# Kernel tuning notes

Measured on AMD Instinct MI355X. Metric: run time of the kernel, lower is better.

Reference implementation:

```python
import jax, jax.numpy as jnp
import numpy as np

T, B, C = 1024, 16, 1024
H, K, PAD_L = 16, 7, 3  # num_heads, kernel_size, padding_l
OUT = 1024


def setup_inputs() -> dict:
    key = jax.random.key(0)
    ks = jax.random.split(key, 8)
    s_in = 1.0 / np.sqrt(C)
    return {
        "x": jax.random.normal(ks[0], (T, B, C), dtype=jnp.float32),
        "W1": jax.random.normal(ks[1], (C, C), dtype=jnp.float32) * s_in,
        "b1": jnp.zeros((C,), dtype=jnp.float32),
        "Wq": jax.random.normal(ks[2], (C, H * K), dtype=jnp.float32) * s_in,
        "bq": jnp.zeros((H * K,), dtype=jnp.float32),
        "conv_bias": jax.random.normal(ks[3], (C,), dtype=jnp.float32) * 0.02,
        "W2": jax.random.normal(ks[4], (C, OUT), dtype=jnp.float32) * s_in,
        "b2": jnp.zeros((OUT,), dtype=jnp.float32),
    }


def reference(x, W1, b1, Wq, bq, conv_bias, W2, b2):
    # linear1 (glu=False -> no activation)
    h = x @ W1 + b1                       # [T, B, C]
    Tn, Bn, Cn = h.shape
    R = Cn // H                           # channels per head
    # dynamic filter prediction from query (= h), softmax over K taps
    w = (h @ Wq + bq).reshape(Tn, Bn, H, K)
    w = jax.nn.softmax(w, axis=-1)        # [T, B, H, K]
    # unfold1d: pad PAD_L left, K-1-PAD_L right along time, gather K-windows
    hp = jnp.pad(h, ((PAD_L, K - 1 - PAD_L), (0, 0), (0, 0)))
    win = jnp.stack([hp[k:k + Tn] for k in range(K)], axis=-1)  # [T, B, C, K]
    win = win.reshape(Tn, Bn, H, R, K)
    out = jnp.einsum('tbhrk,tbhk->tbhr', win, w).reshape(Tn, Bn, Cn)
    out = out + conv_bias                 # [T, B, C]
    return out @ W2 + b2                  # [T, B, OUT]
```

## Files before the change

kernel.cpp:

```cpp
#include <hip/hip_runtime.h>
#include <math.h>

#define T_DIM 1024
#define B_DIM 16
#define C_DIM 1024
#define H_DIM 16
#define K_TAPS 7
#define PAD_LEFT 3
#define OUT_DIM 1024
#define M_DIM (T_DIM * B_DIM)
#define HK 112
#define HKP 128
#define KD 1024
#define NT32 (KD / 32)

typedef __attribute__((ext_vector_type(8))) short bf16x8;
typedef __attribute__((ext_vector_type(4))) float f32x4;

__device__ __forceinline__ ushort f2bf(float f) {
    union { float f; unsigned u; } v; v.f = f;
    unsigned u = v.u;
    u += 0x7fffu + ((u >> 16) & 1u);
    return (ushort)(u >> 16);
}
__device__ __forceinline__ float bf2f(ushort h) {
    union { unsigned u; float f; } v; v.u = ((unsigned)h) << 16;
    return v.f;
}

__global__ __launch_bounds__(256) void cvt_bf16x8(const float* __restrict__ in,
                                                  ushort* __restrict__ out,
                                                  int n8) {
    int i = blockIdx.x * blockDim.x + threadIdx.x;
    if (i >= n8) return;
    const float4* p = (const float4*)in;
    float4 a = p[2 * i], b = p[2 * i + 1];
    uint4 o;
    o.x = (unsigned)f2bf(a.x) | ((unsigned)f2bf(a.y) << 16);
    o.y = (unsigned)f2bf(a.z) | ((unsigned)f2bf(a.w) << 16);
    o.z = (unsigned)f2bf(b.x) | ((unsigned)f2bf(b.y) << 16);
    o.w = (unsigned)f2bf(b.z) | ((unsigned)f2bf(b.w) << 16);
    ((uint4*)out)[i] = o;
}

__global__ void transpose_cvt(const float* __restrict__ W,
                              ushort* __restrict__ Wt,
                              int Kd, int N, int Npad) {
    __shared__ float tile[32][33];
    int n0 = blockIdx.x * 32, k0 = blockIdx.y * 32;
    int tx = threadIdx.x, ty = threadIdx.y;
#pragma unroll
    for (int j = 0; j < 4; ++j) {
        int k = k0 + ty * 4 + j;
        int n = n0 + tx;
        tile[ty * 4 + j][tx] = (n < N) ? W[(size_t)k * N + n] : 0.f;
    }
    __syncthreads();
#pragma unroll
    for (int j = 0; j < 4; ++j) {
        int n = n0 + ty * 4 + j;
        if (n < Npad)
            Wt[(size_t)n * Kd + k0 + tx] = f2bf(tile[tx][ty * 4 + j]);
    }
}

template <bool OUT_BF16>
__global__ __launch_bounds__(256, 2) void gemm_k32(
    const ushort* __restrict__ A, const ushort* __restrict__ Bt,
    const float* __restrict__ bias, void* __restrict__ Cp, int ldc) {
    __shared__ ushort Ab[2][256 * 32];
    __shared__ ushort Bb[2][128 * 32];

    const int tid  = threadIdx.x;
    const int lane = tid & 63;
    const int wid  = tid >> 6;
    const int wr = wid >> 1;
    const int wc = wid & 1;
    const int fr = lane & 15;
    const int fq = lane >> 4;

    const int orig = blockIdx.x;
    const int nid  = (orig & 7) * 64 + (orig >> 3);
    const int bm = (nid >> 3) * 256;
    const int bn = (nid & 7) * 128;

    const int rA   = tid >> 2;
    const int slA  = (tid & 3) * 8;
    const size_t srcA0 = (size_t)(bm + rA) * KD + slA;
    const size_t srcB0 = (size_t)(bn + rA) * KD + slA;

    const int aBase0 = (wr * 128 + fr) * 32 + fq * 8;
    const int bBase0 = (wc * 64 + fr) * 32 + fq * 8;

    f32x4 acc[8][4];
#pragma unroll
    for (int m = 0; m < 8; ++m)
#pragma unroll
        for (int n = 0; n < 4; ++n) acc[m][n] = (f32x4){0.f, 0.f, 0.f, 0.f};

    auto stage = [&](int buf, int t) {
        const ushort* Ap = A + srcA0 + t * 32;
        const ushort* Bp = Bt + srcB0 + t * 32;
#pragma unroll
        for (int i = 0; i < 4; ++i)
            __builtin_amdgcn_global_load_lds(
                (const __attribute__((address_space(1))) void*)(Ap + (size_t)i * 64 * KD),
                (__attribute__((address_space(3))) void*)(&Ab[buf][(i * 256 + wid * 64) * 8]),
                16, 0, 0);
#pragma unroll
        for (int i = 0; i < 2; ++i)
            __builtin_amdgcn_global_load_lds(
                (const __attribute__((address_space(1))) void*)(Bp + (size_t)i * 64 * KD),
                (__attribute__((address_space(3))) void*)(&Bb[buf][(i * 256 + wid * 64) * 8]),
                16, 0, 0);
    };

    stage(0, 0);
    stage(1, 1);
    asm volatile("s_waitcnt vmcnt(6)" ::: "memory");
    __builtin_amdgcn_sched_barrier(0);
    __builtin_amdgcn_s_barrier();

#pragma unroll 1
    for (int t = 0; t < NT32; ++t) {
        const int cur = t & 1;
        const ushort* Ac = &Ab[cur][0];
        const ushort* Bc = &Bb[cur][0];

        bf16x8 a[8], b[4];
#pragma unroll
        for (int n = 0; n < 4; ++n)
            b[n] = *(const bf16x8*)(Bc + bBase0 + n * 512);
#pragma unroll
        for (int m = 0; m < 8; ++m)
            a[m] = *(const bf16x8*)(Ac + aBase0 + m * 512);

        asm volatile("s_waitcnt lgkmcnt(0)" ::: "memory");
        __builtin_amdgcn_sched_barrier(0);
        __builtin_amdgcn_s_barrier();

        if (t < NT32 - 2) stage(cur, t + 2);

        __builtin_amdgcn_s_setprio(1);
#pragma unroll
        for (int m = 0; m < 8; ++m)
#pragma unroll
            for (int n = 0; n < 4; ++n)
                acc[m][n] = __builtin_amdgcn_mfma_f32_16x16x32_bf16(
                    a[m], b[n], acc[m][n], 0, 0, 0);
        __builtin_amdgcn_s_setprio(0);

        if (t < NT32 - 2) {
            asm volatile("s_waitcnt vmcnt(6)" ::: "memory");
        } else if (t == NT32 - 2) {
            asm volatile("s_waitcnt vmcnt(0)" ::: "memory");
        }
        __builtin_amdgcn_sched_barrier(0);
        if (t < NT32 - 1) __builtin_amdgcn_s_barrier();
    }

#pragma unroll
    for (int n = 0; n < 4; ++n) {
        int col = bn + wc * 64 + n * 16 + fr;
        float bv = bias[col];
#pragma unroll
        for (int m = 0; m < 8; ++m) {
#pragma unroll
            for (int r = 0; r < 4; ++r) {
                int row = bm + wr * 128 + m * 16 + fq * 4 + r;
                float v = acc[m][n][r] + bv;
                if (OUT_BF16)
                    ((ushort*)Cp)[(size_t)row * ldc + col] = f2bf(v);
                else
                    ((float*)Cp)[(size_t)row * ldc + col] = v;
            }
        }
    }
}

template <bool OUT_BF16, bool NGUARD>
__global__ __launch_bounds__(256) void gemm_mfma(const ushort* __restrict__ A,
                                                 const ushort* __restrict__ Bt,
                                                 const float* __restrict__ bias,
                                                 void* __restrict__ Cp,
                                                 int Kd, int N, int ldc) {
    __shared__ ushort Als[128 * 32];
    __shared__ ushort Bls[128 * 32];
    const int tid  = threadIdx.x;
    const int lane = tid & 63;
    const int wid  = tid >> 6;
    const int wr = wid >> 1, wc = wid & 1;
    const int bm = blockIdx.y * 128, bn = blockIdx.x * 128;
    const int fq = lane >> 4, fr = lane & 15;

    f32x4 acc[4][4];
#pragma unroll
    for (int m = 0; m < 4; ++m)
#pragma unroll
        for (int n = 0; n < 4; ++n) acc[m][n] = (f32x4){0.f, 0.f, 0.f, 0.f};

    const int c0 = wid * 128 + lane;
    const int c1 = c0 + 64;
    const int r0 = c0 >> 2, o0 = (c0 & 3) * 8;
    const int r1 = c1 >> 2, o1 = (c1 & 3) * 8;

    for (int k0 = 0; k0 < Kd; k0 += 32) {
        __builtin_amdgcn_global_load_lds(
            (const __attribute__((address_space(1))) void*)&A[(size_t)(bm + r0) * Kd + k0 + o0],
            (__attribute__((address_space(3))) void*)&Als[(wid * 2 + 0) * 512], 16, 0, 0);
        __builtin_amdgcn_global_load_lds(
            (const __attribute__((address_space(1))) void*)&A[(size_t)(bm + r1) * Kd + k0 + o1],
            (__attribute__((address_space(3))) void*)&Als[(wid * 2 + 1) * 512], 16, 0, 0);
        __builtin_amdgcn_global_load_lds(
            (const __attribute__((address_space(1))) void*)&Bt[(size_t)(bn + r0) * Kd + k0 + o0],
            (__attribute__((address_space(3))) void*)&Bls[(wid * 2 + 0) * 512], 16, 0, 0);
        __builtin_amdgcn_global_load_lds(
            (const __attribute__((address_space(1))) void*)&Bt[(size_t)(bn + r1) * Kd + k0 + o1],
            (__attribute__((address_space(3))) void*)&Bls[(wid * 2 + 1) * 512], 16, 0, 0);
        __syncthreads();

        bf16x8 af[4], bfr[4];
#pragma unroll
        for (int m = 0; m < 4; ++m)
            af[m] = *(const bf16x8*)&Als[(wr * 64 + m * 16 + fr) * 32 + fq * 8];
#pragma unroll
        for (int n = 0; n < 4; ++n)
            bfr[n] = *(const bf16x8*)&Bls[(wc * 64 + n * 16 + fr) * 32 + fq * 8];
#pragma unroll
        for (int m = 0; m < 4; ++m)
#pragma unroll
            for (int n = 0; n < 4; ++n)
                acc[m][n] = __builtin_amdgcn_mfma_f32_16x16x32_bf16(
                    af[m], bfr[n], acc[m][n], 0, 0, 0);
        __syncthreads();
    }

#pragma unroll
    for (int m = 0; m < 4; ++m) {
#pragma unroll
        for (int n = 0; n < 4; ++n) {
            int col = bn + wc * 64 + n * 16 + fr;
            if (NGUARD && col >= N) continue;
            float bv = bias[col];
#pragma unroll
            for (int r = 0; r < 4; ++r) {
                int row = bm + wr * 64 + m * 16 + fq * 4 + r;
                float v = acc[m][n][r] + bv;
                if (OUT_BF16)
                    ((ushort*)Cp)[(size_t)row * ldc + col] = f2bf(v);
                else
                    ((float*)Cp)[(size_t)row * ldc + col] = v;
            }
        }
    }
}

__global__ __launch_bounds__(256) void dynconv_bf16(const ushort* __restrict__ h,
                                                    const float* __restrict__ q,
                                                    const float* __restrict__ cbias,
                                                    ushort* __restrict__ out) {
    const int m = blockIdx.x;
    const int t = m >> 4;
    const int b = m & 15;

    __shared__ float wsm[HK];
    if (threadIdx.x < HK)
        wsm[threadIdx.x] = q[(size_t)m * HK + threadIdx.x];
    __syncthreads();
    if (threadIdx.x < H_DIM) {
        float* p = &wsm[threadIdx.x * K_TAPS];
        float mx = p[0];
#pragma unroll
        for (int k = 1; k < K_TAPS; ++k) mx = fmaxf(mx, p[k]);
        float e[K_TAPS], s = 0.f;
#pragma unroll
        for (int k = 0; k < K_TAPS; ++k) { e[k] = __expf(p[k] - mx); s += e[k]; }
        float inv = 1.f / s;
#pragma unroll
        for (int k = 0; k < K_TAPS; ++k) p[k] = e[k] * inv;
    }
    __syncthreads();

    const int c = threadIdx.x * 4;
    const int hh = c >> 6;

    float4 bias = *(const float4*)&cbias[c];
    float a0 = bias.x, a1 = bias.y, a2 = bias.z, a3 = bias.w;

#pragma unroll
    for (int k = 0; k < K_TAPS; ++k) {
        int tt = t + k - PAD_LEFT;
        if (tt < 0 || tt >= T_DIM) continue;
        ushort4 hv = *(const ushort4*)&h[((size_t)tt * B_DIM + b) * C_DIM + c];
        float wk = wsm[hh * K_TAPS + k];
        a0 = fmaf(bf2f(hv.x), wk, a0);
        a1 = fmaf(bf2f(hv.y), wk, a1);
        a2 = fmaf(bf2f(hv.z), wk, a2);
        a3 = fmaf(bf2f(hv.w), wk, a3);
    }
    ushort4 o;
    o.x = f2bf(a0); o.y = f2bf(a1); o.z = f2bf(a2); o.w = f2bf(a3);
    *(ushort4*)&out[(size_t)m * C_DIM + c] = o;
}

extern "C" void kernel_launch(void* const* d_in, const int* in_sizes, int n_in,
                              void* d_out, int out_size, void* d_ws,
                              size_t ws_size, hipStream_t stream) {
    const float* x     = (const float*)d_in[0];
    const float* W1    = (const float*)d_in[1];
    const float* b1    = (const float*)d_in[2];
    const float* Wq    = (const float*)d_in[3];
    const float* bq    = (const float*)d_in[4];
    const float* cbias = (const float*)d_in[5];
    const float* W2    = (const float*)d_in[6];
    const float* b2    = (const float*)d_in[7];
    float* out = (float*)d_out;

    ushort* xb    = (ushort*)d_ws;
    ushort* hb    = xb    + (size_t)M_DIM * C_DIM;
    ushort* convb = hb    + (size_t)M_DIM * C_DIM;
    ushort* W1t   = convb + (size_t)M_DIM * C_DIM;
    ushort* W2t   = W1t   + (size_t)C_DIM * C_DIM;
    ushort* Wqt   = W2t   + (size_t)C_DIM * OUT_DIM;
    float*  q     = (float*)(Wqt + (size_t)HKP * C_DIM);

    cvt_bf16x8<<<dim3(M_DIM * C_DIM / 8 / 256), dim3(256), 0, stream>>>(
        x, xb, M_DIM * C_DIM / 8);
    transpose_cvt<<<dim3(C_DIM / 32, C_DIM / 32), dim3(32, 8), 0, stream>>>(
        W1, W1t, C_DIM, C_DIM, C_DIM);
    transpose_cvt<<<dim3(HKP / 32, C_DIM / 32), dim3(32, 8), 0, stream>>>(
        Wq, Wqt, C_DIM, HK, HKP);
    transpose_cvt<<<dim3(OUT_DIM / 32, C_DIM / 32), dim3(32, 8), 0, stream>>>(
        W2, W2t, C_DIM, OUT_DIM, OUT_DIM);

    gemm_k32<true><<<dim3(512), dim3(256), 0, stream>>>(xb, W1t, b1, hb, C_DIM);

    gemm_mfma<false, true>
        <<<dim3(1, M_DIM / 128), dim3(256), 0, stream>>>(
            hb, Wqt, bq, q, C_DIM, HK, HK);

    dynconv_bf16<<<dim3(M_DIM), dim3(256), 0, stream>>>(hb, q, cbias, convb);

    gemm_k32<false><<<dim3(512), dim3(256), 0, stream>>>(convb, W2t, b2, out,
                                                         OUT_DIM);
}
```

Baseline: 171.7 us.

## Replace 256x128 GEMM with 8-wave 256x256 tile, 4-stage swizzled pipeline

Rewrites the two large bf16 GEMMs to use 512-thread blocks computing 256x256 tiles. K-slices are staged into a 4-slot LDS ring with XOR-swizzled layout to avoid bank conflicts. The main loop is split into eight half-tile phases that interleave global-to-LDS loads with MFMA work. It aims to raise data reuse per block and hide load latency, but uses one block per CU, more LDS, and a fragile hand-tuned waitcnt schedule.

```diff
diff --git a/kernel.cpp b/kernel.cpp
--- a/kernel.cpp
+++ b/kernel.cpp
@@ -12,7 +12,6 @@
 #define HK 112
 #define HKP 128
 #define KD 1024
-#define NT32 (KD / 32)
 
 typedef __attribute__((ext_vector_type(8))) short bf16x8;
 typedef __attribute__((ext_vector_type(4))) float f32x4;
@@ -64,33 +63,65 @@
     }
 }
 
+#define PHASE(P2KS, MH, READB, STAGE_STMT, VM_STMT)                           \
+    {                                                                         \
+        if (READB) {                                                          \
+            _Pragma("unroll")                                                 \
+            for (int n = 0; n < 4; ++n)                                       \
+                b[n] = *(const bf16x8*)(Bbase + (P2KS)*8192 + bOff + n*512);  \
+        }                                                                     \
+        bf16x8 a_[4];                                                         \
+        _Pragma("unroll")                                                     \
+        for (int m = 0; m < 4; ++m)                                           \
+            a_[m] = *(const bf16x8*)(Abase + (P2KS)*8192 + aOff +             \
+                                     (MH)*2048 + m*512);                      \
+        STAGE_STMT;                                                           \
+        VM_STMT;                                                              \
+        __builtin_amdgcn_s_barrier();                                         \
+        asm volatile("s_waitcnt lgkmcnt(0)" ::: "memory");                    \
+        __builtin_amdgcn_sched_barrier(0);                                    \
+        __builtin_amdgcn_s_setprio(1);                                        \
+        _Pragma("unroll")                                                     \
+        for (int m = 0; m < 4; ++m)                                           \
+            _Pragma("unroll")                                                 \
+            for (int n = 0; n < 4; ++n)                                       \
+                acc[(MH)*4 + m][n] = __builtin_amdgcn_mfma_f32_16x16x32_bf16( \
+                    a_[m], b[n], acc[(MH)*4 + m][n], 0, 0, 0);                \
+        __builtin_amdgcn_s_setprio(0);                                        \
+        __builtin_amdgcn_s_barrier();                                         \
+        __builtin_amdgcn_sched_barrier(0);                                    \
+    }
+
 template <bool OUT_BF16>
-__global__ __launch_bounds__(256, 2) void gemm_k32(
+__global__ __launch_bounds__(512, 1) void gemm8p(
     const ushort* __restrict__ A, const ushort* __restrict__ Bt,
     const float* __restrict__ bias, void* __restrict__ Cp, int ldc) {
-    __shared__ ushort Ab[2][256 * 32];
-    __shared__ ushort Bb[2][128 * 32];
+    __shared__ ushort Lds[8 * 8192];
 
     const int tid  = threadIdx.x;
     const int lane = tid & 63;
     const int wid  = tid >> 6;
-    const int wr = wid >> 1;
-    const int wc = wid & 1;
+    const int wr = wid >> 2;
+    const int wc = wid & 3;
     const int fr = lane & 15;
     const int fq = lane >> 4;
 
     const int orig = blockIdx.x;
-    const int nid  = (orig & 7) * 64 + (orig >> 3);
-    const int bm = (nid >> 3) * 256;
-    const int bn = (nid & 7) * 128;
-
-    const int rA   = tid >> 2;
-    const int slA  = (tid & 3) * 8;
-    const size_t srcA0 = (size_t)(bm + rA) * KD + slA;
-    const size_t srcB0 = (size_t)(bn + rA) * KD + slA;
-
-    const int aBase0 = (wr * 128 + fr) * 32 + fq * 8;
-    const int bBase0 = (wc * 64 + fr) * 32 + fq * 8;
+    const int nid  = (orig & 7) * 32 + (orig >> 3);
+    const int bm = (nid >> 2) * 256;
+    const int bn = (nid & 3) * 256;
+
+    const int srow = tid >> 2;
+    const int scol = ((tid & 3) ^ ((tid >> 3) & 3)) * 8;
+    const size_t sA = (size_t)(bm + srow) * KD + scol;
+    const size_t sB = (size_t)(bn + srow) * KD + scol;
+    const int sdst = wid * 64 * 8;
+
+    const int slotSw = (fq ^ ((fr >> 1) & 3)) * 8;
+    const int aOff = (wr * 128 + fr) * 32 + slotSw;
+    const int bOff = (wc * 64 + fr) * 32 + slotSw;
+    const ushort* Abase = &Lds[0];
+    const ushort* Bbase = &Lds[4 * 8192];
 
     f32x4 acc[8][4];
 #pragma unroll
@@ -98,65 +129,67 @@
 #pragma unroll
         for (int n = 0; n < 4; ++n) acc[m][n] = (f32x4){0.f, 0.f, 0.f, 0.f};
 
-    auto stage = [&](int buf, int t) {
-        const ushort* Ap = A + srcA0 + t * 32;
-        const ushort* Bp = Bt + srcB0 + t * 32;
-#pragma unroll
-        for (int i = 0; i < 4; ++i)
-            __builtin_amdgcn_global_load_lds(
-                (const __attribute__((address_space(1))) void*)(Ap + (size_t)i * 64 * KD),
-                (__attribute__((address_space(3))) void*)(&Ab[buf][(i * 256 + wid * 64) * 8]),
-                16, 0, 0);
+    auto stageA = [&](int slot, int koff) {
 #pragma unroll
         for (int i = 0; i < 2; ++i)
             __builtin_amdgcn_global_load_lds(
-                (const __attribute__((address_space(1))) void*)(Bp + (size_t)i * 64 * KD),
-                (__attribute__((address_space(3))) void*)(&Bb[buf][(i * 256 + wid * 64) * 8]),
+                (const __attribute__((address_space(1))) void*)(A + sA + koff + (size_t)i * 128 * KD),
+                (__attribute__((address_space(3))) void*)(&Lds[slot * 8192 + i * 4096 + sdst]),
                 16, 0, 0);
     };
-
-    stage(0, 0);
-    stage(1, 1);
-    asm volatile("s_waitcnt vmcnt(6)" ::: "memory");
+    auto stageB = [&](int slot, int koff) {
+#pragma unroll
+        for (int i = 0; i < 2; ++i)
+            __builtin_amdgcn_global_load_lds(
+                (const __attribute__((address_space(1))) void*)(Bt + sB + koff + (size_t)i * 128 * KD),
+                (__attribute__((address_space(3))) void*)(&Lds[(4 + slot) * 8192 + i * 4096 + sdst]),
+                16, 0, 0);
+    };
+
+    stageA(0, 0);   stageB(0, 0);
+    stageA(1, 32);  stageB(1, 32);
+    stageA(2, 64);  stageB(2, 64);
+    stageA(3, 96);  stageB(3, 96);
+    asm volatile("s_waitcnt vmcnt(12)" ::: "memory");
     __builtin_amdgcn_sched_barrier(0);
     __builtin_amdgcn_s_barrier();
+    __builtin_amdgcn_sched_barrier(0);
 
 #pragma unroll 1
-    for (int t = 0; t < NT32; ++t) {
-        const int cur = t & 1;
-        const ushort* Ac = &Ab[cur][0];
-        const ushort* Bc = &Bb[cur][0];
-
-        bf16x8 a[8], b[4];
-#pragma unroll
-        for (int n = 0; n < 4; ++n)
-            b[n] = *(const bf16x8*)(Bc + bBase0 + n * 512);
-#pragma unroll
-        for (int m = 0; m < 8; ++m)
-            a[m] = *(const bf16x8*)(Ac + aBase0 + m * 512);
-
-        asm volatile("s_waitcnt lgkmcnt(0)" ::: "memory");
-        __builtin_amdgcn_sched_barrier(0);
-        __builtin_amdgcn_s_barrier();
-
-        if (t < NT32 - 2) stage(cur, t + 2);
-
-        __builtin_amdgcn_s_setprio(1);
-#pragma unroll
-        for (int m = 0; m < 8; ++m)
-#pragma unroll
-            for (int n = 0; n < 4; ++n)
-                acc[m][n] = __builtin_amdgcn_mfma_f32_16x16x32_bf16(
-                    a[m], b[n], acc[m][n], 0, 0, 0);
-        __builtin_amdgcn_s_setprio(0);
-
-        if (t < NT32 - 2) {
-            asm volatile("s_waitcnt vmcnt(6)" ::: "memory");
-        } else if (t == NT32 - 2) {
-            asm volatile("s_waitcnt vmcnt(0)" ::: "memory");
-        }
-        __builtin_amdgcn_sched_barrier(0);
-        if (t < NT32 - 1) __builtin_amdgcn_s_barrier();
+    for (int j = 0; j < 8; ++j) {
+        bf16x8 b[4];
+        const int e = 2 * j;
+
+        PHASE(0, 0, 1,
+              { if (j >= 1) stageA(3, (e + 1) * 64 + 32); },
+              { asm volatile("s_waitcnt vmcnt(6)" ::: "memory");
+                __builtin_amdgcn_sched_barrier(0); })
+        PHASE(0, 1, 0,
+              { if (j >= 1) stageB(3, (e + 1) * 64 + 32); },
+              (void)0; )
+        PHASE(1, 0, 1,
+              { if (j < 7) stageA(0, (e + 2) * 64); },
+              { if (j == 7) { asm volatile("s_waitcnt vmcnt(4)" ::: "memory"); }
+                else        { asm volatile("s_waitcnt vmcnt(6)" ::: "memory"); }
+                __builtin_amdgcn_sched_barrier(0); })
+        PHASE(1, 1, 0,
+              { if (j < 7) stageB(0, (e + 2) * 64); },
+              (void)0; )
+        PHASE(2, 0, 1,
+              { if (j < 7) stageA(1, (e + 2) * 64 + 32); },
+              { if (j == 7) { asm volatile("s_waitcnt vmcnt(0)" ::: "memory"); }
+                else        { asm volatile("s_waitcnt vmcnt(6)" ::: "memory"); }
+                __builtin_amdgcn_sched_barrier(0); })
+        PHASE(2, 1, 0,
+              { if (j < 7) stageB(1, (e + 2) * 64 + 32); },
+              (void)0; )
+        PHASE(3, 0, 1,
+              { if (j < 7) stageA(2, (e + 3) * 64); },
+              { asm volatile("s_waitcnt vmcnt(6)" ::: "memory");
+                __builtin_amdgcn_sched_barrier(0); })
+        PHASE(3, 1, 0,
+              { if (j < 7) stageB(2, (e + 3) * 64); },
+              (void)0; )
     }
 
 #pragma unroll
@@ -333,7 +366,7 @@
     transpose_cvt<<<dim3(OUT_DIM / 32, C_DIM / 32), dim3(32, 8), 0, stream>>>(
         W2, W2t, C_DIM, OUT_DIM, OUT_DIM);
 
-    gemm_k32<true><<<dim3(512), dim3(256), 0, stream>>>(xb, W1t, b1, hb, C_DIM);
+    gemm8p<true><<<dim3(256), dim3(512), 0, stream>>>(xb, W1t, b1, hb, C_DIM);
 
     gemm_mfma<false, true>
         <<<dim3(1, M_DIM / 128), dim3(256), 0, stream>>>(
@@ -341,6 +374,6 @@
 
     dynconv_bf16<<<dim3(M_DIM), dim3(256), 0, stream>>>(hb, q, cbias, convb);
 
-    gemm_k32<false><<<dim3(512), dim3(256), 0, stream>>>(convb, W2t, b2, out,
-                                                         OUT_DIM);
-}
+    gemm8p<false><<<dim3(256), dim3(512), 0, stream>>>(convb, W2t, b2, out,
+                                                       OUT_DIM);
+}
```

Measured after the change: 166.0 us. -3.3%, faster.
